# Performance work log

Hardware: AMD Instinct MI355X
Metric: run time of the kernel (lower is better)

## Reference

```python
import jax, jax.numpy as jnp
import numpy as np

D_MODEL = 1024
HEAD_SIZE = 64
BLOCK_SIZE = 2048
B, T = 4, 2048


def setup_inputs() -> dict:
    key = jax.random.key(0)
    ks = jax.random.split(key, 7)
    s = 1.0 / np.sqrt(D_MODEL)
    x = jax.random.normal(ks[0], (B, T, D_MODEL), dtype=jnp.float32)
    Wq = jax.random.uniform(ks[1], (D_MODEL, HEAD_SIZE), jnp.float32, -s, s)
    bq = jax.random.uniform(ks[2], (HEAD_SIZE,), jnp.float32, -s, s)
    Wk = jax.random.uniform(ks[3], (D_MODEL, HEAD_SIZE), jnp.float32, -s, s)
    bk = jax.random.uniform(ks[4], (HEAD_SIZE,), jnp.float32, -s, s)
    Wv = jax.random.uniform(ks[5], (D_MODEL, HEAD_SIZE), jnp.float32, -s, s)
    return {"x": x, "Wq": Wq, "bq": bq, "Wk": Wk, "bk": bk, "Wv": Wv, "mask": 1}


def reference(x, Wq, bq, Wk, bk, Wv, mask):
    # x: [B, T, C]; single attention head, dropout is identity (eval/p=0)
    Tlen = x.shape[1]
    q = x @ Wq + bq              # [B, T, hs]
    k = x @ Wk + bk              # [B, T, hs]
    v = x @ Wv                   # [B, T, hs] (no bias)
    hs = k.shape[-1]
    # Faithful to source: weights = QK^T / hs**(-0.5)  ==  QK^T * sqrt(hs)
    w = jnp.einsum('btd,bsd->bts', q, k) * jnp.sqrt(jnp.asarray(hs, x.dtype))
    if mask:
        causal = jnp.tril(jnp.ones((Tlen, Tlen), dtype=bool))
        w = jnp.where(causal, w, jnp.asarray(-jnp.inf, w.dtype))
    w = jax.nn.softmax(w, axis=-1)
    out = jnp.einsum('bts,bsd->btd', w, v)  # [B, T, hs]
    return out
```

## Files before the change

kernel.cpp:

```cpp
#include <hip/hip_runtime.h>
#include <hip/hip_bf16.h>

#define D_MODEL 1024
#define HS 64
#define T_LEN 2048
#define JCH 512
#define NCH 4

typedef __attribute__((ext_vector_type(8))) short bf16x8;
typedef __attribute__((ext_vector_type(4))) float f32x4;

__device__ inline void split8(const float* v, int4& hi, int4& lo) {
    union { unsigned short u[8]; int4 v4; } uh, ul;
    #pragma unroll
    for (int i = 0; i < 8; ++i) {
        const unsigned int b = __float_as_uint(v[i]);
        const unsigned short h = (unsigned short)(b >> 16);
        const float r = v[i] - __uint_as_float((unsigned int)h << 16);
        uh.u[i] = h;
        ul.u[i] = (unsigned short)(__float_as_uint(r) >> 16);
    }
    hi = uh.v4; lo = ul.v4;
}

__device__ inline unsigned short f2bf_rne(float f) {
    const unsigned int b = __float_as_uint(f);
    return (unsigned short)((b + 0x7FFFu + ((b >> 16) & 1u)) >> 16);
}
__device__ inline float bf2f(unsigned short h) {
    return __uint_as_float((unsigned int)h << 16);
}

__global__ __launch_bounds__(256) void wprep_kernel(
    const float* __restrict__ Wq, const float* __restrict__ Wk,
    const float* __restrict__ Wv, short* __restrict__ Wh, short* __restrict__ Wl)
{
    __shared__ float tile[64][69];
    const int tid = threadIdx.x;
    const int kb = blockIdx.x & 15;
    const int m  = blockIdx.x >> 4;
    const float* W = (m == 0) ? Wq : (m == 1) ? Wk : Wv;
    #pragma unroll
    for (int it = 0; it < 4; ++it) {
        const int idx = tid + 256 * it;
        const int kr = idx >> 4, c4 = idx & 15;
        *(float4*)&tile[kr][4 * c4] =
            *(const float4*)(W + (size_t)(kb * 64 + kr) * HS + 4 * c4);
    }
    __syncthreads();
    #pragma unroll
    for (int it = 0; it < 2; ++it) {
        const int s = tid + 256 * it;
        const int n = s >> 3, kc = s & 7;
        float v[8];
        #pragma unroll
        for (int i = 0; i < 8; ++i) v[i] = tile[kc * 8 + i][n];
        int4 hi, lo;
        split8(v, hi, lo);
        const size_t off = (size_t)(m * 64 + n) * D_MODEL + kb * 64 + kc * 8;
        *(int4*)(Wh + off) = hi;
        *(int4*)(Wl + off) = lo;
    }
}

__global__ __launch_bounds__(256) void qkv_kernel(
    const float* __restrict__ x,
    const short* __restrict__ Wh, const short* __restrict__ Wl,
    const float* __restrict__ bq, const float* __restrict__ bk,
    float* __restrict__ q, float* __restrict__ k, float* __restrict__ vt, int BT)
{
    __shared__ __align__(16) short Ah[4 * 520], Al[4 * 520];
    __shared__ __align__(16) short Bh[12 * 520], Bl[12 * 520];

    const int tid  = threadIdx.x;
    const int r0   = blockIdx.x * 64;
    const int wave = tid >> 6;
    const int lane = tid & 63;
    const int wn0  = wave * 3;

    f32x4 acc[4][3];
    #pragma unroll
    for (int mt = 0; mt < 4; ++mt)
        #pragma unroll
        for (int j = 0; j < 3; ++j) acc[mt][j] = (f32x4)(0.f);

    const int sm  = tid & 63;
    const int skc = tid >> 6;

    for (int k0 = 0; k0 < D_MODEL; k0 += 32) {
        __syncthreads();
        {
            const float* src = x + (size_t)(r0 + sm) * D_MODEL + k0 + skc * 8;
            float xv[8];
            *(float4*)&xv[0] = *(const float4*)src;
            *(float4*)&xv[4] = *(const float4*)(src + 4);
            int4 hi, lo;
            split8(xv, hi, lo);
            const int mt   = sm >> 4;
            const int slot = (skc << 4) | (sm & 15);
            *(int4*)&Ah[mt * 520 + slot * 8] = hi;
            *(int4*)&Al[mt * 520 + slot * 8] = lo;
        }
        #pragma unroll
        for (int i = 0; i < 3; ++i) {
            const int s   = tid + 256 * i;
            const int nt  = s >> 6;
            const int sl  = s & 63;
            const int kc  = sl >> 4;
            const int nn  = sl & 15;
            const size_t off = (size_t)(nt * 16 + nn) * D_MODEL + k0 + kc * 8;
            *(int4*)&Bh[nt * 520 + sl * 8] = *(const int4*)(Wh + off);
            *(int4*)&Bl[nt * 520 + sl * 8] = *(const int4*)(Wl + off);
        }
        __syncthreads();

        bf16x8 afh[4], afl[4];
        #pragma unroll
        for (int mt = 0; mt < 4; ++mt) {
            afh[mt] = *(const bf16x8*)&Ah[mt * 520 + lane * 8];
            afl[mt] = *(const bf16x8*)&Al[mt * 520 + lane * 8];
        }
        #pragma unroll
        for (int j = 0; j < 3; ++j) {
            const int nt = wn0 + j;
            const bf16x8 bfh = *(const bf16x8*)&Bh[nt * 520 + lane * 8];
            const bf16x8 bfl = *(const bf16x8*)&Bl[nt * 520 + lane * 8];
            #pragma unroll
            for (int mt = 0; mt < 4; ++mt) {
                acc[mt][j] = __builtin_amdgcn_mfma_f32_16x16x32_bf16(afh[mt], bfh, acc[mt][j], 0, 0, 0);
                acc[mt][j] = __builtin_amdgcn_mfma_f32_16x16x32_bf16(afh[mt], bfl, acc[mt][j], 0, 0, 0);
                acc[mt][j] = __builtin_amdgcn_mfma_f32_16x16x32_bf16(afl[mt], bfh, acc[mt][j], 0, 0, 0);
            }
        }
    }

    #pragma unroll
    for (int j = 0; j < 3; ++j) {
        const int c = (wn0 + j) * 16 + (lane & 15);
        #pragma unroll
        for (int mt = 0; mt < 4; ++mt) {
            const int rowb = r0 + mt * 16 + (lane >> 4) * 4;
            if (c < 64) {
                const float bias = bq[c];
                #pragma unroll
                for (int r = 0; r < 4; ++r)
                    q[(size_t)(rowb + r) * HS + c] = acc[mt][j][r] + bias;
            } else if (c < 128) {
                const float bias = bk[c - 64];
                #pragma unroll
                for (int r = 0; r < 4; ++r)
                    k[(size_t)(rowb + r) * HS + (c - 64)] = acc[mt][j][r] + bias;
            } else {
                float4 o;
                o.x = acc[mt][j][0]; o.y = acc[mt][j][1];
                o.z = acc[mt][j][2]; o.w = acc[mt][j][3];
                *(float4*)(vt + (size_t)(c - 128) * BT + rowb) = o;
            }
        }
    }
}

__global__ __launch_bounds__(256) void attn_kernel(
    const float* __restrict__ q_ws, const float* __restrict__ k_ws,
    const float* __restrict__ vt_ws, const int* __restrict__ maskp,
    float* __restrict__ part_O, float* __restrict__ part_ml, int BT)
{
    __shared__ __align__(16) short Kh[4096], Kl[4096];
    __shared__ __align__(16) short Vt[4096];
    __shared__ __align__(16) short Pl[4][16 * 72];

    const int tile  = blockIdx.x;
    const int chunk = blockIdx.y;
    const int r0 = tile * 64;
    const int tb = r0 / T_LEN;
    const int t0 = r0 - tb * T_LEN;
    const int mask = (*maskp != 0);
    const int n_max = mask ? (t0 + 64) : T_LEN;
    const int j0 = chunk * JCH;
    if (j0 >= n_max) return;
    const int hi_j = min(j0 + JCH, n_max);
    const int njt = (hi_j - j0 + 63) >> 6;

    const int tid  = threadIdx.x;
    const int w    = tid >> 6;
    const int lane = tid & 63;
    const int quad = lane >> 4;
    const int l15  = lane & 15;
    const int rw0  = t0 + 16 * w;
    const int rowa = r0 + 16 * w + quad * 4;

    bf16x8 qfh[2], qfl[2];
    {
        const float* qrow = q_ws + (size_t)(r0 + 16 * w + l15) * HS + quad * 8;
        #pragma unroll
        for (int kc = 0; kc < 2; ++kc) {
            float v[8];
            *(float4*)&v[0] = *(const float4*)(qrow + kc * 32);
            *(float4*)&v[4] = *(const float4*)(qrow + kc * 32 + 4);
            union { int4 i; bf16x8 b; } ch, cl;
            split8(v, ch.i, cl.i);
            qfh[kc] = ch.b;
            qfl[kc] = cl.b;
        }
    }

    f32x4 oacc[4];
    #pragma unroll
    for (int nt = 0; nt < 4; ++nt) oacc[nt] = (f32x4)(0.f);
    float m_r[4] = {-INFINITY, -INFINITY, -INFINITY, -INFINITY};
    float l_r[4] = {0.f, 0.f, 0.f, 0.f};

    const float* kbase = k_ws + (size_t)tb * T_LEN * HS;

    for (int jt = 0; jt < njt; ++jt) {
        const int jbase = j0 + jt * 64;
        __syncthreads();
        #pragma unroll
        for (int it = 0; it < 2; ++it) {
            const int s  = tid + 256 * it;
            const int ls = s & 63;
            const int sc = s >> 6;
            const int jsub = sc >> 1, kc = sc & 1;
            const int jrow = jbase + jsub * 16 + (ls & 15);
            const int koff = kc * 32 + (ls >> 4) * 8;
            const float* src = kbase + (size_t)jrow * HS + koff;
            float v[8];
            *(float4*)&v[0] = *(const float4*)src;
            *(float4*)&v[4] = *(const float4*)(src + 4);
            int4 hi, lo;
            split8(v, hi, lo);
            *(int4*)&Kh[s * 8] = hi;
            *(int4*)&Kl[s * 8] = lo;
        }
        #pragma unroll
        for (int it = 0; it < 2; ++it) {
            const int s  = tid + 256 * it;
            const int ls = s & 63;
            const int sc = s >> 6;
            const int jc = sc >> 2, nt = sc & 3;
            const int n  = nt * 16 + (ls & 15);
            const int jcol = jbase + jc * 32 + (ls >> 4) * 8;
            const float* src = vt_ws + (size_t)n * BT + tb * T_LEN + jcol;
            float v[8];
            *(float4*)&v[0] = *(const float4*)src;
            *(float4*)&v[4] = *(const float4*)(src + 4);
            union { unsigned short u[8]; int4 i; } pk;
            #pragma unroll
            for (int i = 0; i < 8; ++i) pk.u[i] = f2bf_rne(v[i]);
            *(int4*)&Vt[s * 8] = pk.i;
        }
        __syncthreads();

        const bool active = (!mask) || (jbase <= rw0 + 15);
        if (active) {
            f32x4 sacc[4];
            #pragma unroll
            for (int jsub = 0; jsub < 4; ++jsub) {
                f32x4 s = (f32x4)(0.f);
                #pragma unroll
                for (int kc = 0; kc < 2; ++kc) {
                    const bf16x8 kh = *(const bf16x8*)&Kh[((jsub * 2 + kc) * 64 + lane) * 8];
                    const bf16x8 kl = *(const bf16x8*)&Kl[((jsub * 2 + kc) * 64 + lane) * 8];
                    s = __builtin_amdgcn_mfma_f32_16x16x32_bf16(qfh[kc], kh, s, 0, 0, 0);
                    s = __builtin_amdgcn_mfma_f32_16x16x32_bf16(qfh[kc], kl, s, 0, 0, 0);
                    s = __builtin_amdgcn_mfma_f32_16x16x32_bf16(qfl[kc], kh, s, 0, 0, 0);
                }
                sacc[jsub] = s;
            }
            float sval[4][4], rmax[4];
            #pragma unroll
            for (int r = 0; r < 4; ++r) rmax[r] = -INFINITY;
            #pragma unroll
            for (int jsub = 0; jsub < 4; ++jsub) {
                const int jg = jbase + jsub * 16 + l15;
                #pragma unroll
                for (int r = 0; r < 4; ++r) {
                    const int tg = rw0 + quad * 4 + r;
                    const float vv = (mask && (jg > tg)) ? -INFINITY : 8.0f * sacc[jsub][r];
                    sval[jsub][r] = vv;
                    rmax[r] = fmaxf(rmax[r], vv);
                }
            }
            #pragma unroll
            for (int d = 1; d < 16; d <<= 1)
                #pragma unroll
                for (int r = 0; r < 4; ++r)
                    rmax[r] = fmaxf(rmax[r], __shfl_xor(rmax[r], d));
            float alpha[4], msafe[4];
            #pragma unroll
            for (int r = 0; r < 4; ++r) {
                const float mn = fmaxf(m_r[r], rmax[r]);
                msafe[r] = (mn == -INFINITY) ? 0.f : mn;
                alpha[r] = __expf(m_r[r] - msafe[r]);
                m_r[r] = mn;
            }
            short* Pw = &Pl[w][0];
            float rsum[4] = {0.f, 0.f, 0.f, 0.f};
            #pragma unroll
            for (int jsub = 0; jsub < 4; ++jsub) {
                #pragma unroll
                for (int r = 0; r < 4; ++r) {
                    const float e = __expf(sval[jsub][r] - msafe[r]);
                    const unsigned short eb = f2bf_rne(e);
                    Pw[(quad * 4 + r) * 72 + jsub * 16 + l15] = (short)eb;
                    rsum[r] += bf2f(eb);
                }
            }
            #pragma unroll
            for (int d = 1; d < 16; d <<= 1)
                #pragma unroll
                for (int r = 0; r < 4; ++r)
                    rsum[r] += __shfl_xor(rsum[r], d);
            #pragma unroll
            for (int r = 0; r < 4; ++r)
                l_r[r] = l_r[r] * alpha[r] + rsum[r];
            #pragma unroll
            for (int nt = 0; nt < 4; ++nt)
                #pragma unroll
                for (int r = 0; r < 4; ++r)
                    oacc[nt][r] *= alpha[r];
            bf16x8 pf[2];
            #pragma unroll
            for (int jc = 0; jc < 2; ++jc)
                pf[jc] = *(const bf16x8*)&Pw[l15 * 72 + jc * 32 + quad * 8];
            #pragma unroll
            for (int nt = 0; nt < 4; ++nt) {
                #pragma unroll
                for (int jc = 0; jc < 2; ++jc) {
                    const bf16x8 vf = *(const bf16x8*)&Vt[((jc * 4 + nt) * 64 + lane) * 8];
                    oacc[nt] = __builtin_amdgcn_mfma_f32_16x16x32_bf16(pf[jc], vf, oacc[nt], 0, 0, 0);
                }
            }
        }
    }

    #pragma unroll
    for (int nt = 0; nt < 4; ++nt)
        #pragma unroll
        for (int r = 0; r < 4; ++r)
            part_O[((size_t)(rowa + r) * NCH + chunk) * HS + nt * 16 + l15] = oacc[nt][r];
    if (l15 == 0) {
        #pragma unroll
        for (int r = 0; r < 4; ++r) {
            float2 ml;
            ml.x = m_r[r];
            ml.y = l_r[r];
            *(float2*)(part_ml + ((size_t)(rowa + r) * NCH + chunk) * 2) = ml;
        }
    }
}

__global__ __launch_bounds__(256) void combine_kernel(
    const float* __restrict__ part_O, const float* __restrict__ part_ml,
    const int* __restrict__ maskp, float* __restrict__ out)
{
    const int f = blockIdx.x * 256 + threadIdx.x;
    const int row = f >> 6;
    const int d = f & 63;
    const int t = row & (T_LEN - 1);
    const int mask = (*maskp != 0);
    const int n = mask ? (t + 1) : T_LEN;
    const int nc = (n + JCH - 1) / JCH;

    float mv[NCH], lv[NCH];
    float M = -INFINITY;
    for (int c = 0; c < nc; ++c) {
        const float2 ml = *(const float2*)(part_ml + ((size_t)row * NCH + c) * 2);
        mv[c] = ml.x; lv[c] = ml.y;
        M = fmaxf(M, ml.x);
    }
    float L = 0.f, O = 0.f;
    for (int c = 0; c < nc; ++c) {
        const float w = __expf(mv[c] - M);
        L += lv[c] * w;
        O = fmaf(part_O[((size_t)row * NCH + c) * HS + d], w, O);
    }
    out[(size_t)row * HS + d] = O / L;
}

extern "C" void kernel_launch(void* const* d_in, const int* in_sizes, int n_in,
                              void* d_out, int out_size, void* d_ws, size_t ws_size,
                              hipStream_t stream) {
    const float* x  = (const float*)d_in[0];
    const float* Wq = (const float*)d_in[1];
    const float* bq = (const float*)d_in[2];
    const float* Wk = (const float*)d_in[3];
    const float* bk = (const float*)d_in[4];
    const float* Wv = (const float*)d_in[5];
    const int* maskp = (const int*)d_in[6];

    const int BT = in_sizes[0] / D_MODEL;

    float* q   = (float*)d_ws;
    float* k   = q + (size_t)BT * HS;
    float* vt  = k + (size_t)BT * HS;
    float* pO  = vt + (size_t)BT * HS;
    float* pml = pO + (size_t)BT * NCH * HS;

    short* Wh = (short*)pO;
    short* Wl = Wh + (size_t)192 * D_MODEL;

    wprep_kernel<<<48, 256, 0, stream>>>(Wq, Wk, Wv, Wh, Wl);
    qkv_kernel<<<BT / 64, 256, 0, stream>>>(x, Wh, Wl, bq, bk, q, k, vt, BT);
    dim3 agrid(BT / 64, NCH);
    attn_kernel<<<agrid, 256, 0, stream>>>(q, k, vt, maskp, pO, pml, BT);
    combine_kernel<<<(BT * HS) / 256, 256, 0, stream>>>(pO, pml, maskp, (float*)d_out);
}
```

Before: 171.0 us.

## Split QKV projection into smaller tiles and prefetch next k-step loads

The QKV projection now uses 32-row tiles and splits the 192 output columns across two blocks per row tile, launching four times as many blocks with a lighter per-block register footprint (launch bounds request 2 blocks per CU). Global loads for the next k-step are issued into registers before the MFMA work of the current step, overlapping memory latency with compute. The aim is to fill more compute units, since the old grid had fewer blocks than CUs. The cost is that x is read once per column half, doubling its global traffic, and each wave gets less MFMA reuse per LDS load.

```diff
diff --git a/kernel.cpp b/kernel.cpp
--- a/kernel.cpp
+++ b/kernel.cpp
@@ -63,99 +63,118 @@
     }
 }
 
-__global__ __launch_bounds__(256) void qkv_kernel(
+__global__ __launch_bounds__(256, 2) void qkv_kernel(
     const float* __restrict__ x,
     const short* __restrict__ Wh, const short* __restrict__ Wl,
     const float* __restrict__ bq, const float* __restrict__ bk,
     float* __restrict__ q, float* __restrict__ k, float* __restrict__ vt, int BT)
 {
-    __shared__ __align__(16) short Ah[4 * 520], Al[4 * 520];
-    __shared__ __align__(16) short Bh[12 * 520], Bl[12 * 520];
+    __shared__ __align__(16) short Ah[2 * 520], Al[2 * 520];
+    __shared__ __align__(16) short Bh[6 * 520], Bl[6 * 520];
 
     const int tid  = threadIdx.x;
-    const int r0   = blockIdx.x * 64;
+    const int r0   = blockIdx.x * 32;
+    const int nb   = blockIdx.y;
     const int wave = tid >> 6;
     const int lane = tid & 63;
-    const int wn0  = wave * 3;
-
-    f32x4 acc[4][3];
-    #pragma unroll
-    for (int mt = 0; mt < 4; ++mt)
-        #pragma unroll
-        for (int j = 0; j < 3; ++j) acc[mt][j] = (f32x4)(0.f);
-
-    const int sm  = tid & 63;
-    const int skc = tid >> 6;
+    const int mt_w = wave >> 1;
+    const int nt0  = (wave & 1) * 3;
+
+    f32x4 acc[3];
+    #pragma unroll
+    for (int j = 0; j < 3; ++j) acc[j] = (f32x4)(0.f);
+
+    const bool doA = (tid >= 128);
+    const int  au  = tid & 127;
+    const int  amt = au >> 6;
+    const int  aln = au & 63;
+    const float* axsrc =
+        x + (size_t)(r0 + amt * 16 + (aln & 15)) * D_MODEL + (aln >> 4) * 8;
+
+    const int b0nt = tid >> 6;
+    const int b0ln = tid & 63;
+    const size_t b0off =
+        (size_t)(nb * 96 + b0nt * 16 + (b0ln & 15)) * D_MODEL + (b0ln >> 4) * 8;
+    const int b1nt = 4 + (tid >> 6);
+    const int b1ln = tid & 63;
+    const size_t b1off =
+        (size_t)(nb * 96 + b1nt * 16 + (b1ln & 15)) * D_MODEL + (b1ln >> 4) * 8;
+
+    float4 a0v, a1v;
+    int4 b0h, b0l, b1h, b1l;
+    if (doA) {
+        a0v = *(const float4*)(axsrc);
+        a1v = *(const float4*)(axsrc + 4);
+    }
+    b0h = *(const int4*)(Wh + b0off);
+    b0l = *(const int4*)(Wl + b0off);
+    if (!doA) {
+        b1h = *(const int4*)(Wh + b1off);
+        b1l = *(const int4*)(Wl + b1off);
+    }
 
     for (int k0 = 0; k0 < D_MODEL; k0 += 32) {
         __syncthreads();
-        {
-            const float* src = x + (size_t)(r0 + sm) * D_MODEL + k0 + skc * 8;
+        if (doA) {
             float xv[8];
-            *(float4*)&xv[0] = *(const float4*)src;
-            *(float4*)&xv[4] = *(const float4*)(src + 4);
+            *(float4*)&xv[0] = a0v;
+            *(float4*)&xv[4] = a1v;
             int4 hi, lo;
             split8(xv, hi, lo);
-            const int mt   = sm >> 4;
-            const int slot = (skc << 4) | (sm & 15);
-            *(int4*)&Ah[mt * 520 + slot * 8] = hi;
-            *(int4*)&Al[mt * 520 + slot * 8] = lo;
-        }
-        #pragma unroll
-        for (int i = 0; i < 3; ++i) {
-            const int s   = tid + 256 * i;
-            const int nt  = s >> 6;
-            const int sl  = s & 63;
-            const int kc  = sl >> 4;
-            const int nn  = sl & 15;
-            const size_t off = (size_t)(nt * 16 + nn) * D_MODEL + k0 + kc * 8;
-            *(int4*)&Bh[nt * 520 + sl * 8] = *(const int4*)(Wh + off);
-            *(int4*)&Bl[nt * 520 + sl * 8] = *(const int4*)(Wl + off);
+            *(int4*)&Ah[amt * 520 + aln * 8] = hi;
+            *(int4*)&Al[amt * 520 + aln * 8] = lo;
+        }
+        *(int4*)&Bh[b0nt * 520 + b0ln * 8] = b0h;
+        *(int4*)&Bl[b0nt * 520 + b0ln * 8] = b0l;
+        if (!doA) {
+            *(int4*)&Bh[b1nt * 520 + b1ln * 8] = b1h;
+            *(int4*)&Bl[b1nt * 520 + b1ln * 8] = b1l;
         }
         __syncthreads();
-
-        bf16x8 afh[4], afl[4];
-        #pragma unroll
-        for (int mt = 0; mt < 4; ++mt) {
-            afh[mt] = *(const bf16x8*)&Ah[mt * 520 + lane * 8];
-            afl[mt] = *(const bf16x8*)&Al[mt * 520 + lane * 8];
-        }
+        const int kn = k0 + 32;
+        if (kn < D_MODEL) {
+            if (doA) {
+                a0v = *(const float4*)(axsrc + kn);
+                a1v = *(const float4*)(axsrc + kn + 4);
+            }
+            b0h = *(const int4*)(Wh + b0off + kn);
+            b0l = *(const int4*)(Wl + b0off + kn);
+            if (!doA) {
+                b1h = *(const int4*)(Wh + b1off + kn);
+                b1l = *(const int4*)(Wl + b1off + kn);
+            }
+        }
+        const bf16x8 afh = *(const bf16x8*)&Ah[mt_w * 520 + lane * 8];
+        const bf16x8 afl = *(const bf16x8*)&Al[mt_w * 520 + lane * 8];
         #pragma unroll
         for (int j = 0; j < 3; ++j) {
-            const int nt = wn0 + j;
+            const int nt = nt0 + j;
             const bf16x8 bfh = *(const bf16x8*)&Bh[nt * 520 + lane * 8];
             const bf16x8 bfl = *(const bf16x8*)&Bl[nt * 520 + lane * 8];
-            #pragma unroll
-            for (int mt = 0; mt < 4; ++mt) {
-                acc[mt][j] = __builtin_amdgcn_mfma_f32_16x16x32_bf16(afh[mt], bfh, acc[mt][j], 0, 0, 0);
-                acc[mt][j] = __builtin_amdgcn_mfma_f32_16x16x32_bf16(afh[mt], bfl, acc[mt][j], 0, 0, 0);
-                acc[mt][j] = __builtin_amdgcn_mfma_f32_16x16x32_bf16(afl[mt], bfh, acc[mt][j], 0, 0, 0);
-            }
-        }
-    }
-
+            acc[j] = __builtin_amdgcn_mfma_f32_16x16x32_bf16(afh, bfh, acc[j], 0, 0, 0);
+            acc[j] = __builtin_amdgcn_mfma_f32_16x16x32_bf16(afh, bfl, acc[j], 0, 0, 0);
+            acc[j] = __builtin_amdgcn_mfma_f32_16x16x32_bf16(afl, bfh, acc[j], 0, 0, 0);
+        }
+    }
+
+    const int rowb = r0 + mt_w * 16 + (lane >> 4) * 4;
     #pragma unroll
     for (int j = 0; j < 3; ++j) {
-        const int c = (wn0 + j) * 16 + (lane & 15);
-        #pragma unroll
-        for (int mt = 0; mt < 4; ++mt) {
-            const int rowb = r0 + mt * 16 + (lane >> 4) * 4;
-            if (c < 64) {
-                const float bias = bq[c];
-                #pragma unroll
-                for (int r = 0; r < 4; ++r)
-                    q[(size_t)(rowb + r) * HS + c] = acc[mt][j][r] + bias;
-            } else if (c < 128) {
-                const float bias = bk[c - 64];
-                #pragma unroll
-                for (int r = 0; r < 4; ++r)
-                    k[(size_t)(rowb + r) * HS + (c - 64)] = acc[mt][j][r] + bias;
-            } else {
-                float4 o;
-                o.x = acc[mt][j][0]; o.y = acc[mt][j][1];
-                o.z = acc[mt][j][2]; o.w = acc[mt][j][3];
-                *(float4*)(vt + (size_t)(c - 128) * BT + rowb) = o;
-            }
+        const int c = nb * 96 + (nt0 + j) * 16 + (lane & 15);
+        if (c < 64) {
+            const float bias = bq[c];
+            #pragma unroll
+            for (int r = 0; r < 4; ++r)
+                q[(size_t)(rowb + r) * HS + c] = acc[j][r] + bias;
+        } else if (c < 128) {
+            const float bias = bk[c - 64];
+            #pragma unroll
+            for (int r = 0; r < 4; ++r)
+                k[(size_t)(rowb + r) * HS + (c - 64)] = acc[j][r] + bias;
+        } else {
+            float4 o;
+            o.x = acc[j][0]; o.y = acc[j][1]; o.z = acc[j][2]; o.w = acc[j][3];
+            *(float4*)(vt + (size_t)(c - 128) * BT + rowb) = o;
         }
     }
 }
@@ -401,7 +420,8 @@
     short* Wl = Wh + (size_t)192 * D_MODEL;
 
     wprep_kernel<<<48, 256, 0, stream>>>(Wq, Wk, Wv, Wh, Wl);
-    qkv_kernel<<<BT / 64, 256, 0, stream>>>(x, Wh, Wl, bq, bk, q, k, vt, BT);
+    dim3 qgrid(BT / 32, 2);
+    qkv_kernel<<<qgrid, 256, 0, stream>>>(x, Wh, Wl, bq, bk, q, k, vt, BT);
     dim3 agrid(BT / 64, NCH);
     attn_kernel<<<agrid, 256, 0, stream>>>(q, k, vt, maskp, pO, pml, BT);
     combine_kernel<<<(BT * HS) / 256, 256, 0, stream>>>(pO, pml, maskp, (float*)d_out);
```

Measured after the change: 156.0 us. 8.8% less time.
